# Kernel optimization log

Hardware: AMD Instinct MI355X
Metric: run time of the kernel (lower is better)

## Reference

```python
import jax, jax.numpy as jnp
import numpy as np
from jax import lax

B, S = 32, 256
V, D = 32000, 300   # pretrained word embeddings
P, PD = 35, 32      # pos vocab / pos embed dim (from source)
M = 66              # morph feature dim
H = 6               # LSTM units per direction -> bilstm_output_size = 12
A = 12


def _lstm(x, Wx, Wh, b, reverse=False):
    # x: [B,S,F] -> h: [B,S,H]; keras gate order i,f,c,o
    xg = x @ Wx + b  # precompute input projection once: [B,S,4H]
    def step(carry, xt):
        h, c = carry
        g = xt + h @ Wh
        i, f, cand, o = jnp.split(g, 4, axis=-1)
        c = jax.nn.sigmoid(f) * c + jax.nn.sigmoid(i) * jnp.tanh(cand)
        h = jax.nn.sigmoid(o) * jnp.tanh(c)
        return (h, c), h
    h0 = jnp.zeros((x.shape[0], Wh.shape[0]), x.dtype)
    _, hs = lax.scan(step, (h0, h0), jnp.swapaxes(xg, 0, 1), reverse=reverse)
    return jnp.swapaxes(hs, 0, 1)


def setup_inputs() -> dict:
    key = jax.random.key(0)
    ks = jax.random.split(key, 16)
    F = D + PD + M
    n = lambda k, shp, s=0.1: jax.random.normal(k, shp, dtype=jnp.float32) * s
    return {
        'words': jax.random.randint(ks[0], (B, S), 0, V),
        'pos': jax.random.randint(ks[1], (B, S), 0, P),
        'morph': jax.random.uniform(ks[2], (B, S, M), dtype=jnp.float32),
        'heads': jax.random.randint(ks[3], (B, S), 0, S),
        'word_table': n(ks[4], (V, D)),
        'pos_table': n(ks[5], (P, PD)),
        'Wx_f': n(ks[6], (F, 4 * H)), 'Wh_f': n(ks[7], (H, 4 * H)), 'b_f': jnp.zeros((4 * H,), jnp.float32),
        'Wx_b': n(ks[8], (F, 4 * H)), 'Wh_b': n(ks[9], (H, 4 * H)), 'b_b': jnp.zeros((4 * H,), jnp.float32),
        'Wu': n(ks[10], (A, A)), 'bu': jnp.zeros((A,), jnp.float32),
        'Ww': n(ks[11], (A, A)), 'bw': jnp.zeros((A,), jnp.float32),
        'v': n(ks[12], (A,)),
    }


def reference(words, pos, morph, heads, word_table, pos_table,
              Wx_f, Wh_f, b_f, Wx_b, Wh_b, b_b, Wu, bu, Ww, bw, v):
    # embed + concat -> [B,S,F]
    feats = jnp.concatenate([word_table[words], pos_table[pos], morph], axis=-1)
    # BiLSTM encoder -> [B,S,12] (dropout disabled / eval)
    hf = _lstm(feats, Wx_f, Wh_f, b_f)
    hb = _lstm(feats, Wx_b, Wh_b, b_b, reverse=True)
    repr_ = jnp.concatenate([hf, hb], axis=-1)
    # Bahdanau arc scoring, vectorized over dependant i (the tf loop):
    # scores[b,i,j] = v . tanh(u_a(repr)[b,j] + w_a(repr)[b,i])
    ua = repr_ @ Wu + bu  # head-position term (j)
    wa = repr_ @ Ww + bw  # dependant term (i)
    scores = jnp.einsum('bijd,d->bij', jnp.tanh(ua[:, None, :, :] + wa[:, :, None, :]), v)
    # the equality-based mask in tf picks out j == i (self cannot be head)
    eye = jnp.eye(S, dtype=bool)
    scores = jnp.where(eye[None], -10000.0, scores)
    # per-step sparse CE (from_logits, mean over batch), summed over i=1..S-1
    logp = jax.nn.log_softmax(scores, axis=-1)
    ce = -jnp.take_along_axis(logp, heads[:, :, None], axis=2)[..., 0]  # [B,S]
    loss = jnp.sum(jnp.mean(ce[:, 1:], axis=0))
    # parent_prob_table: exp(scores) concatenated along axis 0, i-major as in tf loop
    table = jnp.swapaxes(jnp.exp(scores[:, 1:, :]), 0, 1).reshape((S - 1) * B, S)
    return loss, table
```

## Files before the change

### kernel.cpp

```cpp
#include <hip/hip_runtime.h>
#include <hip/hip_bf16.h>

#define BB 32
#define SS 256
#define DD 300
#define PDD 32
#define MM 66
#define FF 398
#define HH 6
#define G4 24
#define AA 12
#define L2E 1.4426950408889634f

__device__ __forceinline__ float fast_rcp(float x) { return __builtin_amdgcn_rcpf(x); }
__device__ __forceinline__ float fast_tanh(float x) {
    return 1.f - 2.f * fast_rcp(__expf(2.f * x) + 1.f);
}
__device__ __forceinline__ float bcast_lane(float x, int l) {
    return __int_as_float(__builtin_amdgcn_readlane(__float_as_int(x), l));
}
template<int CTRL>
__device__ __forceinline__ float quad_bcast(float v) {
    return __int_as_float(__builtin_amdgcn_mov_dpp(__float_as_int(v), CTRL, 0xf, 0xf, true));
}

#define EPB 32
__global__ __launch_bounds__(256) void k_embed_proj(
    const int* __restrict__ words, const int* __restrict__ pos,
    const float* __restrict__ morph, const float* __restrict__ wtab,
    const float* __restrict__ ptab,
    const float* __restrict__ Wxf, const float* __restrict__ bfv,
    const float* __restrict__ Wxb, const float* __restrict__ bbv,
    float* __restrict__ xgf, float* __restrict__ xgb)
{
    __shared__ float4 sF[100][33];
    __shared__ float4 sW[48 * 100];
    int t  = threadIdx.x;
    int p0 = blockIdx.x * EPB;

    for (int idx = t; idx < EPB * 75; idx += 256) {
        int p = idx / 75, q = idx % 75;
        sF[q][p] = *(const float4*)(wtab + (size_t)words[p0 + p] * DD + 4 * q);
    }
    {
        int idx = t;
        int p = idx / 8, q = idx % 8;
        sF[75 + q][p] = *(const float4*)(ptab + pos[p0 + p] * PDD + 4 * q);
    }
    for (int idx = t; idx < EPB * 17; idx += 256) {
        int p = idx / 17, mq = idx % 17;
        const float2* ms = (const float2*)(morph + (size_t)(p0 + p) * MM);
        float2 lo = ms[2 * mq];
        float2 hi = (mq < 16) ? ms[2 * mq + 1] : make_float2(0.f, 0.f);
        sF[83 + mq][p] = make_float4(lo.x, lo.y, hi.x, hi.y);
    }
    {
        float* sWf = (float*)sW;
        for (int idx = t; idx < FF * G4; idx += 256) {
            int k = idx / G4, j = idx % G4;
            sWf[j * 400 + k]        = Wxf[idx];
            sWf[(24 + j) * 400 + k] = Wxb[idx];
        }
        if (t < 2 * G4) {
            int j = t >> 1, k = 398 + (t & 1);
            sWf[j * 400 + k] = 0.f; sWf[(24 + j) * 400 + k] = 0.f;
        }
    }
    __syncthreads();

    int lane = t & 63, w = t >> 6;
    int p    = lane & 31;
    int cg   = w * 2 + (lane >> 5);
    int dir  = cg >> 2;
    int tg   = cg & 3;
    int j0   = tg * 6;
    const float4* wc = sW + (dir * 24 + j0) * 100;

    float a0 = 0.f, a1 = 0.f, a2 = 0.f, a3 = 0.f, a4 = 0.f, a5 = 0.f;
    #pragma unroll 4
    for (int q = 0; q < 100; ++q) {
        float4 f = sF[q][p];
        float4 w0 = wc[0 * 100 + q], w1 = wc[1 * 100 + q], w2 = wc[2 * 100 + q];
        float4 w3 = wc[3 * 100 + q], w4 = wc[4 * 100 + q], w5 = wc[5 * 100 + q];
        a0 = fmaf(f.x, w0.x, a0); a0 = fmaf(f.y, w0.y, a0);
        a0 = fmaf(f.z, w0.z, a0); a0 = fmaf(f.w, w0.w, a0);
        a1 = fmaf(f.x, w1.x, a1); a1 = fmaf(f.y, w1.y, a1);
        a1 = fmaf(f.z, w1.z, a1); a1 = fmaf(f.w, w1.w, a1);
        a2 = fmaf(f.x, w2.x, a2); a2 = fmaf(f.y, w2.y, a2);
        a2 = fmaf(f.z, w2.z, a2); a2 = fmaf(f.w, w2.w, a2);
        a3 = fmaf(f.x, w3.x, a3); a3 = fmaf(f.y, w3.y, a3);
        a3 = fmaf(f.z, w3.z, a3); a3 = fmaf(f.w, w3.w, a3);
        a4 = fmaf(f.x, w4.x, a4); a4 = fmaf(f.y, w4.y, a4);
        a4 = fmaf(f.z, w4.z, a4); a4 = fmaf(f.w, w4.w, a4);
        a5 = fmaf(f.x, w5.x, a5); a5 = fmaf(f.y, w5.y, a5);
        a5 = fmaf(f.z, w5.z, a5); a5 = fmaf(f.w, w5.w, a5);
    }

    float kk = (tg == 2) ? 2.f * L2E : -L2E;
    const float* bias = dir ? bbv : bfv;
    float* o = (dir ? xgb : xgf) + (size_t)(p0 + p) * G4 + j0;
    o[0] = (a0 + bias[j0 + 0]) * kk; o[1] = (a1 + bias[j0 + 1]) * kk;
    o[2] = (a2 + bias[j0 + 2]) * kk; o[3] = (a3 + bias[j0 + 3]) * kk;
    o[4] = (a4 + bias[j0 + 4]) * kk; o[5] = (a5 + bias[j0 + 5]) * kk;
}

__global__ __launch_bounds__(128) void k_lstm_uawa(
    const float* __restrict__ xgf, const float* __restrict__ xgb,
    const float* __restrict__ Whf, const float* __restrict__ Whb,
    const float* __restrict__ Wu, const float* __restrict__ bu,
    const float* __restrict__ Ww, const float* __restrict__ bw,
    float* __restrict__ ua, float* __restrict__ wa)
{
    __shared__ float sxg[2][(SS + 8) * G4];
    __shared__ float hbuf[2][SS * HH];
    int b    = blockIdx.x;
    int lane = threadIdx.x & 63;
    int dir  = __builtin_amdgcn_readfirstlane(threadIdx.x >> 6);

    const float* xg = (dir ? xgb : xgf) + (size_t)b * SS * G4;
    const float* Wh = dir ? Whb : Whf;

    {
        const float4* src = (const float4*)xg;
        float4* dst = (float4*)sxg[dir];
        #pragma unroll
        for (int u = 0; u < 24; ++u) {
            int d = lane + u * 64;
            int row = d / 6, c4 = d - row * 6;
            int drow = dir ? (SS - 1 - row) : row;
            dst[drow * 6 + c4] = src[d];
        }
        for (int g2 = lane; g2 < 8 * G4; g2 += 64) sxg[dir][SS * G4 + g2] = 0.f;
    }

    int g    = lane % G4;
    int cell = g >> 2;
    int type = g & 3;
    int j    = type * HH + cell;

    float kk = (type == 2) ? 2.f * L2E : -L2E;
    float wh[HH];
    #pragma unroll
    for (int m = 0; m < HH; ++m) wh[m] = Wh[m * G4 + j] * kk;
    float Bc = (type == 2) ? 1.f : 0.f;
    float Ac = (type == 2) ? -1.f : 1.f;

    float sh[HH];
    #pragma unroll
    for (int m = 0; m < HH; ++m) sh[m] = 0.f;
    float c = 0.f;
    bool wr = (lane < G4) && ((lane & 3) == 0);

    const float* xb = sxg[dir] + j;
    float* hb = hbuf[dir];

    float pg[4];
    #pragma unroll
    for (int sl = 0; sl < 4; ++sl) pg[sl] = xb[sl * G4];

    #pragma unroll 1
    for (int t = 0; t < SS; t += 4) {
        #pragma unroll
        for (int sl = 0; sl < 4; ++sl) {
            float x = pg[sl];
            pg[sl] = xb[(t + 4 + sl) * G4];

            float aa  = fmaf(sh[1], wh[1], fmaf(sh[0], wh[0], x));
            float bb2 = fmaf(sh[3], wh[3], sh[2] * wh[2]);
            float cc2 = fmaf(sh[5], wh[5], sh[4] * wh[4]);
            x = (aa + bb2) + cc2;

            float e   = __builtin_amdgcn_exp2f(x);
            float val = fmaf(Bc, e, Ac) * fast_rcp(1.f + e);

            float vi = quad_bcast<0>(val);
            float vf = quad_bcast<85>(val);
            float vc = quad_bcast<170>(val);
            float vo = quad_bcast<255>(val);

            c = fmaf(vf, c, vi * vc);
            float ec = __builtin_amdgcn_exp2f(c * (2.f * L2E));
            float h  = (ec - 1.f) * fast_rcp(ec + 1.f) * vo;

            if (wr) hb[(t + sl) * HH + cell] = h;
            #pragma unroll
            for (int m = 0; m < HH; ++m) sh[m] = bcast_lane(h, 4 * m);
        }
    }
    __syncthreads();

    #pragma unroll
    for (int half = 0; half < 2; ++half) {
        int s = (int)threadIdx.x + half * 128;
        float r[AA];
        #pragma unroll
        for (int cc = 0; cc < HH; ++cc) {
            r[cc]      = hbuf[0][s * HH + cc];
            r[HH + cc] = hbuf[1][(SS - 1 - s) * HH + cc];
        }
        float au[AA], aw[AA];
        #pragma unroll
        for (int d = 0; d < AA; ++d) { au[d] = bu[d]; aw[d] = bw[d]; }
        #pragma unroll
        for (int e2 = 0; e2 < AA; ++e2) {
            #pragma unroll
            for (int d = 0; d < AA; ++d) {
                au[d] = fmaf(r[e2], Wu[e2 * AA + d], au[d]);
                aw[d] = fmaf(r[e2], Ww[e2 * AA + d], aw[d]);
            }
        }
        float* ou = ua + ((size_t)b * SS + s) * AA;
        float* ow = wa + ((size_t)b * SS + s) * AA;
        #pragma unroll
        for (int d4 = 0; d4 < 3; ++d4) {
            *(float4*)(ou + 4 * d4) = make_float4(au[4*d4], au[4*d4+1], au[4*d4+2], au[4*d4+3]);
            *(float4*)(ow + 4 * d4) = make_float4(aw[4*d4], aw[4*d4+1], aw[4*d4+2], aw[4*d4+3]);
        }
    }
}

__global__ __launch_bounds__(256) void k_score(
    const float* __restrict__ ua, const float* __restrict__ wa,
    const float* __restrict__ v, const int* __restrict__ heads,
    float* __restrict__ out, float* __restrict__ ce)
{
    int bi = blockIdx.x;
    int i  = bi & 255;
    int j  = threadIdx.x;

    __shared__ float swa[AA], sv[AA];
    if (j < AA) { swa[j] = wa[(size_t)bi * AA + j]; sv[j] = v[j]; }
    __syncthreads();

    const float* uj = ua + ((size_t)(bi & ~255) + j) * AA;
    float s = 0.f;
    #pragma unroll
    for (int d = 0; d < AA; ++d) s = fmaf(sv[d], fast_tanh(uj[d] + swa[d]), s);
    if (j == i) s = -10000.f;

    float e = __expf(s);
    if (i >= 1)
        out[1 + (((size_t)(i - 1) * BB + (bi >> 8)) * SS + j)] = e;

    float r = e;
    #pragma unroll
    for (int off = 32; off > 0; off >>= 1) r += __shfl_xor(r, off, 64);
    __shared__ float part[4];
    if ((j & 63) == 0) part[j >> 6] = r;
    __syncthreads();
    float tot = part[0] + part[1] + part[2] + part[3];

    if (j == heads[bi])
        ce[bi] = (i >= 1) ? (__logf(tot) - s) : 0.f;
}

__global__ __launch_bounds__(256) void k_loss(const float* __restrict__ ce,
                                              float* __restrict__ out)
{
    __shared__ float red[256];
    int t = threadIdx.x;
    float a = 0.f;
    for (int k = t; k < BB * SS; k += 256) a += ce[k];
    red[t] = a; __syncthreads();
    for (int off = 128; off > 0; off >>= 1) {
        if (t < off) red[t] += red[t + off];
        __syncthreads();
    }
    if (t == 0) out[0] = red[0] * (1.f / BB);
}

extern "C" void kernel_launch(void* const* d_in, const int* in_sizes, int n_in,
                              void* d_out, int out_size, void* d_ws, size_t ws_size,
                              hipStream_t stream)
{
    const int*   words = (const int*)  d_in[0];
    const int*   pos   = (const int*)  d_in[1];
    const float* morph = (const float*)d_in[2];
    const int*   heads = (const int*)  d_in[3];
    const float* wtab  = (const float*)d_in[4];
    const float* ptab  = (const float*)d_in[5];
    const float* Wxf   = (const float*)d_in[6];
    const float* Whf   = (const float*)d_in[7];
    const float* bf    = (const float*)d_in[8];
    const float* Wxb   = (const float*)d_in[9];
    const float* Whb   = (const float*)d_in[10];
    const float* bb    = (const float*)d_in[11];
    const float* Wu    = (const float*)d_in[12];
    const float* bu    = (const float*)d_in[13];
    const float* Ww    = (const float*)d_in[14];
    const float* bw    = (const float*)d_in[15];
    const float* v     = (const float*)d_in[16];
    float* out = (float*)d_out;

    float* xgf  = (float*)d_ws;
    float* xgb  = xgf  + (size_t)BB*SS*G4;
    float* ua   = xgb  + (size_t)BB*SS*G4;
    float* wa   = ua   + (size_t)BB*SS*AA;
    float* ce   = wa   + (size_t)BB*SS*AA;

    k_embed_proj<<<(BB * SS) / EPB, 256, 0, stream>>>(words, pos, morph, wtab, ptab,
                                                      Wxf, bf, Wxb, bb, xgf, xgb);
    k_lstm_uawa<<<BB, 128, 0, stream>>>(xgf, xgb, Whf, Whb, Wu, bu, Ww, bw, ua, wa);
    k_score<<<BB * SS, 256, 0, stream>>>(ua, wa, v, heads, out, ce);
    k_loss<<<1, 256, 0, stream>>>(ce, out);
}
```

Before: 74.15 us.

## Pre-transpose LSTM input weights once and batch four dependants per score block

A tiny new kernel transposes Wx_f/Wx_b into a padded global layout once, so each embed-projection block reads weights from global/L2 instead of restaging 77KB of shared memory per block. This cuts the per-block setup cost and shared-memory footprint, which may let more blocks share a CU, at the price of global loads in the inner loop. The score kernel now handles four dependant rows per block. Each thread reuses its loaded ua row across those rows and the launch count drops fourfold. The tanh is rewritten algebraically as sum(v) - 2*sum(v*sigmoid), with the 2*log2(e) scale folded into ua/wa, so each term needs only one exp2 and one reciprocal.

```diff
diff --git a/kernel.cpp b/kernel.cpp
--- a/kernel.cpp
+++ b/kernel.cpp
@@ -13,28 +13,40 @@
 #define L2E 1.4426950408889634f
 
 __device__ __forceinline__ float fast_rcp(float x) { return __builtin_amdgcn_rcpf(x); }
-__device__ __forceinline__ float fast_tanh(float x) {
-    return 1.f - 2.f * fast_rcp(__expf(2.f * x) + 1.f);
-}
 __device__ __forceinline__ float bcast_lane(float x, int l) {
     return __int_as_float(__builtin_amdgcn_readlane(__float_as_int(x), l));
 }
 template<int CTRL>
 __device__ __forceinline__ float quad_bcast(float v) {
     return __int_as_float(__builtin_amdgcn_mov_dpp(__float_as_int(v), CTRL, 0xf, 0xf, true));
+}
+
+__global__ __launch_bounds__(256) void k_wtprep(
+    const float* __restrict__ Wxf, const float* __restrict__ Wxb,
+    float* __restrict__ WT)
+{
+    const float* Wx = blockIdx.x ? Wxb : Wxf;
+    float* wt = WT + blockIdx.x * (G4 * 400);
+    int t = threadIdx.x;
+    for (int idx = t; idx < FF * G4; idx += 256) {
+        int k = idx / G4, j = idx % G4;
+        wt[j * 400 + k] = Wx[idx];
+    }
+    if (t < 2 * G4) {
+        int j = t >> 1, k = 398 + (t & 1);
+        wt[j * 400 + k] = 0.f;
+    }
 }
 
 #define EPB 32
 __global__ __launch_bounds__(256) void k_embed_proj(
     const int* __restrict__ words, const int* __restrict__ pos,
     const float* __restrict__ morph, const float* __restrict__ wtab,
-    const float* __restrict__ ptab,
-    const float* __restrict__ Wxf, const float* __restrict__ bfv,
-    const float* __restrict__ Wxb, const float* __restrict__ bbv,
+    const float* __restrict__ ptab, const float* __restrict__ WT,
+    const float* __restrict__ bfv, const float* __restrict__ bbv,
     float* __restrict__ xgf, float* __restrict__ xgb)
 {
     __shared__ float4 sF[100][33];
-    __shared__ float4 sW[48 * 100];
     int t  = threadIdx.x;
     int p0 = blockIdx.x * EPB;
 
@@ -54,18 +66,6 @@
         float2 hi = (mq < 16) ? ms[2 * mq + 1] : make_float2(0.f, 0.f);
         sF[83 + mq][p] = make_float4(lo.x, lo.y, hi.x, hi.y);
     }
-    {
-        float* sWf = (float*)sW;
-        for (int idx = t; idx < FF * G4; idx += 256) {
-            int k = idx / G4, j = idx % G4;
-            sWf[j * 400 + k]        = Wxf[idx];
-            sWf[(24 + j) * 400 + k] = Wxb[idx];
-        }
-        if (t < 2 * G4) {
-            int j = t >> 1, k = 398 + (t & 1);
-            sWf[j * 400 + k] = 0.f; sWf[(24 + j) * 400 + k] = 0.f;
-        }
-    }
     __syncthreads();
 
     int lane = t & 63, w = t >> 6;
@@ -74,7 +74,7 @@
     int dir  = cg >> 2;
     int tg   = cg & 3;
     int j0   = tg * 6;
-    const float4* wc = sW + (dir * 24 + j0) * 100;
+    const float4* wc = (const float4*)(WT + (size_t)(dir * G4 + j0) * 400);
 
     float a0 = 0.f, a1 = 0.f, a2 = 0.f, a3 = 0.f, a4 = 0.f, a5 = 0.f;
     #pragma unroll 4
@@ -213,8 +213,10 @@
         float* ow = wa + ((size_t)b * SS + s) * AA;
         #pragma unroll
         for (int d4 = 0; d4 < 3; ++d4) {
-            *(float4*)(ou + 4 * d4) = make_float4(au[4*d4], au[4*d4+1], au[4*d4+2], au[4*d4+3]);
-            *(float4*)(ow + 4 * d4) = make_float4(aw[4*d4], aw[4*d4+1], aw[4*d4+2], aw[4*d4+3]);
+            *(float4*)(ou + 4 * d4) = make_float4(au[4*d4] * (2.f*L2E), au[4*d4+1] * (2.f*L2E),
+                                                  au[4*d4+2] * (2.f*L2E), au[4*d4+3] * (2.f*L2E));
+            *(float4*)(ow + 4 * d4) = make_float4(aw[4*d4] * (2.f*L2E), aw[4*d4+1] * (2.f*L2E),
+                                                  aw[4*d4+2] * (2.f*L2E), aw[4*d4+3] * (2.f*L2E));
         }
     }
 }
@@ -224,34 +226,61 @@
     const float* __restrict__ v, const int* __restrict__ heads,
     float* __restrict__ out, float* __restrict__ ce)
 {
-    int bi = blockIdx.x;
-    int i  = bi & 255;
-    int j  = threadIdx.x;
-
-    __shared__ float swa[AA], sv[AA];
-    if (j < AA) { swa[j] = wa[(size_t)bi * AA + j]; sv[j] = v[j]; }
+    int blk = blockIdx.x;
+    int b   = blk >> 6;
+    int i0  = (blk & 63) * 4;
+    int j   = threadIdx.x;
+    int w   = j >> 6;
+
+    __shared__ float swa[4][AA], sv[AA];
+    __shared__ float part[4][4];
+    if (j < 4 * AA) swa[j / AA][j % AA] = wa[((size_t)b * SS + i0 + j / AA) * AA + j % AA];
+    if (j < AA) sv[j] = v[j];
     __syncthreads();
 
-    const float* uj = ua + ((size_t)(bi & ~255) + j) * AA;
-    float s = 0.f;
-    #pragma unroll
-    for (int d = 0; d < AA; ++d) s = fmaf(sv[d], fast_tanh(uj[d] + swa[d]), s);
-    if (j == i) s = -10000.f;
-
-    float e = __expf(s);
-    if (i >= 1)
-        out[1 + (((size_t)(i - 1) * BB + (bi >> 8)) * SS + j)] = e;
-
-    float r = e;
-    #pragma unroll
-    for (int off = 32; off > 0; off >>= 1) r += __shfl_xor(r, off, 64);
-    __shared__ float part[4];
-    if ((j & 63) == 0) part[j >> 6] = r;
+    float sumv = 0.f;
+    #pragma unroll
+    for (int d = 0; d < AA; ++d) sumv += sv[d];
+
+    const float* uj = ua + ((size_t)b * SS + j) * AA;
+    float4 u0 = *(const float4*)(uj);
+    float4 u1 = *(const float4*)(uj + 4);
+    float4 u2 = *(const float4*)(uj + 8);
+    float us[AA] = {u0.x, u0.y, u0.z, u0.w, u1.x, u1.y, u1.z, u1.w,
+                    u2.x, u2.y, u2.z, u2.w};
+
+    float sv_[4];
+    #pragma unroll
+    for (int ii = 0; ii < 4; ++ii) {
+        int i = i0 + ii;
+        float acc = 0.f;
+        #pragma unroll
+        for (int d = 0; d < AA; ++d) {
+            float e_d = __builtin_amdgcn_exp2f(us[d] + swa[ii][d]);
+            acc = fmaf(sv[d], fast_rcp(1.f + e_d), acc);
+        }
+        float s = fmaf(-2.f, acc, sumv);
+        if (j == i) s = -10000.f;
+        sv_[ii] = s;
+
+        float e = __builtin_amdgcn_exp2f(s * L2E);
+        if (i >= 1)
+            out[1 + (((size_t)(i - 1) * BB + b) * SS + j)] = e;
+
+        float r = e;
+        #pragma unroll
+        for (int off = 32; off > 0; off >>= 1) r += __shfl_xor(r, off, 64);
+        if ((j & 63) == 0) part[ii][w] = r;
+    }
     __syncthreads();
-    float tot = part[0] + part[1] + part[2] + part[3];
-
-    if (j == heads[bi])
-        ce[bi] = (i >= 1) ? (__logf(tot) - s) : 0.f;
+
+    #pragma unroll
+    for (int ii = 0; ii < 4; ++ii) {
+        int i = i0 + ii;
+        float tot = part[ii][0] + part[ii][1] + part[ii][2] + part[ii][3];
+        if (j == heads[b * SS + i])
+            ce[b * SS + i] = (i >= 1) ? (__logf(tot) - sv_[ii]) : 0.f;
+    }
 }
 
 __global__ __launch_bounds__(256) void k_loss(const float* __restrict__ ce,
@@ -297,10 +326,12 @@
     float* ua   = xgb  + (size_t)BB*SS*G4;
     float* wa   = ua   + (size_t)BB*SS*AA;
     float* ce   = wa   + (size_t)BB*SS*AA;
-
+    float* WT   = ce   + (size_t)BB*SS;
+
+    k_wtprep<<<2, 256, 0, stream>>>(Wxf, Wxb, WT);
     k_embed_proj<<<(BB * SS) / EPB, 256, 0, stream>>>(words, pos, morph, wtab, ptab,
-                                                      Wxf, bf, Wxb, bb, xgf, xgb);
+                                                      WT, bf, bb, xgf, xgb);
     k_lstm_uawa<<<BB, 128, 0, stream>>>(xgf, xgb, Whf, Whb, Wu, bu, Ww, bw, ua, wa);
-    k_score<<<BB * SS, 256, 0, stream>>>(ua, wa, v, heads, out, ce);
+    k_score<<<BB * (SS / 4), 256, 0, stream>>>(ua, wa, v, heads, out, ce);
     k_loss<<<1, 256, 0, stream>>>(ce, out);
 }
```

Result: slower. 96.22 us (+29.8%).
